# Optimization experiments

Measured on AMD Instinct MI355X. Metric: run time of the kernel, lower is better.

The kernel has to match this reference:

```python
import jax, jax.numpy as jnp
import numpy as np

NEG_INF = -9e15  # matches torch's -9000000000000000.0 mask value
ALPHA = 0.2      # LeakyReLU negative slope


def setup_inputs() -> dict:
    key = jax.random.key(0)
    k1, k2, k3, k4 = jax.random.split(key, 4)
    B, N, Fin, Fout = 8, 2048, 256, 256
    h = jax.random.normal(k1, (B, N, Fin), dtype=jnp.float32)
    adj = jax.random.randint(k2, (B, N, N), 0, 2, dtype=jnp.int32)
    # xavier_uniform with gain=1.414
    limW = 1.414 * np.sqrt(6.0 / (Fin + Fout))
    W = jax.random.uniform(k3, (Fin, Fout), minval=-limW, maxval=limW, dtype=jnp.float32)
    lima = 1.414 * np.sqrt(6.0 / (2 * Fout + 1))
    a = jax.random.uniform(k4, (2 * Fout, 1), minval=-lima, maxval=lima, dtype=jnp.float32)
    return {"h": h, "adj": adj, "W": W, "a": a}


def reference(h, adj, W, a):
    # h: (B, N, Fin), adj: (B, N, N), W: (Fin, Fout), a: (2*Fout, 1)
    Fout = W.shape[1]
    Wh = jnp.einsum('bni,io->bno', h, W)                 # (B, N, Fout)
    # e[b,i,j] = leakyrelu(Wh[b,i] @ a1 + Wh[b,j] @ a2) -- equivalent to the
    # original concat([Wh_i, Wh_j]) @ a without the O(N^2 * 2F) intermediate.
    e1 = Wh @ a[:Fout, 0]                                # (B, N)
    e2 = Wh @ a[Fout:, 0]                                # (B, N)
    e = jax.nn.leaky_relu(e1[:, :, None] + e2[:, None, :], negative_slope=ALPHA)
    masked = jnp.where(adj > 0, e, NEG_INF)
    attention = jax.nn.softmax(masked, axis=-1)          # (B, N, N)
    # dropout omitted (deterministic eval-mode reference)
    h_prime = jnp.einsum('bij,bjo->bio', attention, Wh)  # (B, N, Fout)
    return jax.nn.elu(h_prime), attention
```

## Files before the change

kernel.cpp:

```cpp
#include <hip/hip_runtime.h>
#include <hip/hip_bf16.h>
#include <stdint.h>

#define NEG_INF -9.0e15f
#define LRELU_ALPHA 0.2f
#define LOG2E 1.442695040888963f

using bf16x8  = __attribute__((ext_vector_type(8))) short;
using f32x4   = __attribute__((ext_vector_type(4))) float;
using short4v = __attribute__((ext_vector_type(4))) short;
using int4v   = __attribute__((ext_vector_type(4))) int;
using float4v = __attribute__((ext_vector_type(4))) float;
using uint2v  = __attribute__((ext_vector_type(2))) unsigned;
using uint4v  = __attribute__((ext_vector_type(4))) unsigned;

static __device__ __forceinline__ short f2bf(float f) {
  unsigned u = __builtin_bit_cast(unsigned, f);
  u = u + 0x7FFFu + ((u >> 16) & 1u);
  return (short)(u >> 16);
}
static __device__ __forceinline__ unsigned cvtpk_bf16(float lo, float hi) {
  unsigned r;
  asm volatile("v_cvt_pk_bf16_f32 %0, %1, %2" : "=v"(r) : "v"(lo), "v"(hi));
  return r;
}
static __device__ __forceinline__ void gload16(const void* g, void* l) {
  __builtin_amdgcn_global_load_lds((const __attribute__((address_space(1))) void*)g,
                                   (__attribute__((address_space(3))) void*)l, 16, 0, 0);
}

__global__ __launch_bounds__(256) void prep_kernel(
    const float* __restrict__ W, const float* __restrict__ a,
    short* __restrict__ W_t, float* __restrict__ aW1, float* __restrict__ aW2)
{
  const int bid = blockIdx.x;
  const int tid = threadIdx.x;
  if (bid < 16) {
    __shared__ float t[64][65];
    const int m0 = (bid & 3) * 64, n0 = (bid >> 2) * 64;
    const int rr = tid >> 3, cc = (tid & 7) * 8;
#pragma unroll
    for (int p = 0; p < 2; ++p) {
      int row = rr + p * 32;
      const float* sp = W + (m0 + row) * 256 + n0 + cc;
      float4v v0 = *(const float4v*)sp;
      float4v v1 = *(const float4v*)(sp + 4);
#pragma unroll
      for (int j = 0; j < 4; ++j) { t[row][cc + j] = v0[j]; t[row][cc + 4 + j] = v1[j]; }
    }
    __syncthreads();
#pragma unroll
    for (int p = 0; p < 2; ++p) {
      int orow = rr + p * 32;
      short vv[8] __attribute__((aligned(16)));
#pragma unroll
      for (int j = 0; j < 8; ++j) vv[j] = f2bf(t[cc + j][orow]);
      short* dp = W_t + (n0 + orow) * 256 + m0 + cc;
      *(int4v*)dp = *(const int4v*)vv;
    }
  } else {
    const int r8 = tid >> 3, o4 = (tid & 7) * 4;
    float s1[8] = {}, s2[8] = {};
#pragma unroll
    for (int rp = 0; rp < 8; ++rp) {
      int row = r8 + rp * 32;
#pragma unroll
      for (int k = 0; k < 8; ++k) {
        int o = o4 + k * 32;
        float4v wv = *(const float4v*)(W + row * 256 + o);
        float4v a1 = *(const float4v*)(a + o);
        float4v a2 = *(const float4v*)(a + 256 + o);
#pragma unroll
        for (int e = 0; e < 4; ++e) { s1[rp] += wv[e] * a1[e]; s2[rp] += wv[e] * a2[e]; }
      }
    }
#pragma unroll
    for (int rp = 0; rp < 8; ++rp) {
#pragma unroll
      for (int off = 4; off > 0; off >>= 1) {
        s1[rp] += __shfl_xor(s1[rp], off, 64);
        s2[rp] += __shfl_xor(s2[rp], off, 64);
      }
      if ((tid & 7) == 0) { aW1[r8 + rp * 32] = s1[rp]; aW2[r8 + rp * 32] = s2[rp]; }
    }
  }
}

__global__ __launch_bounds__(256) void gemm_h_kernel(
    const float* __restrict__ A, const short* __restrict__ Bt,
    short* __restrict__ Wht, const float* __restrict__ aW1,
    const float* __restrict__ aW2, float* __restrict__ e1, float* __restrict__ e2)
{
  __shared__ short As[128 * 32];
  __shared__ short Bs[128 * 32];
  __shared__ short T[128][136];
  const int m0 = blockIdx.x * 128, n0 = blockIdx.y * 128;
  const int tid = threadIdx.x;
  const int w = tid >> 6, lane = tid & 63;
  const int wr = w >> 1, wc = w & 1;
  const int g = lane >> 4, lr = lane & 15;
  const bool doE = (blockIdx.y == 0);

  f32x4 acc[4][4] = {};
  float s1q[2] = {0.f, 0.f}, s2q[2] = {0.f, 0.f};

  for (int k0 = 0; k0 < 256; k0 += 32) {
    __syncthreads();
#pragma unroll
    for (int q = 0; q < 2; ++q) {
      int c = q * 256 + tid;
      int row = c >> 2, kq = (c & 3) << 3;
      const float* ap = A + (long long)(m0 + row) * 256 + k0 + kq;
      float4v u0 = *(const float4v*)ap;
      float4v u1 = *(const float4v*)(ap + 4);
      if (doE) {
        float4v w1a = *(const float4v*)(aW1 + k0 + kq);
        float4v w1b = *(const float4v*)(aW1 + k0 + kq + 4);
        float4v w2a = *(const float4v*)(aW2 + k0 + kq);
        float4v w2b = *(const float4v*)(aW2 + k0 + kq + 4);
#pragma unroll
        for (int e = 0; e < 4; ++e) {
          s1q[q] += u0[e] * w1a[e] + u1[e] * w1b[e];
          s2q[q] += u0[e] * w2a[e] + u1[e] * w2b[e];
        }
      }
      uint4v uv;
      uv[0] = cvtpk_bf16(u0[0], u0[1]);
      uv[1] = cvtpk_bf16(u0[2], u0[3]);
      uv[2] = cvtpk_bf16(u1[0], u1[1]);
      uv[3] = cvtpk_bf16(u1[2], u1[3]);
      *(bf16x8*)(As + c * 8) = __builtin_bit_cast(bf16x8, uv);
    }
#pragma unroll
    for (int q = 0; q < 2; ++q) {
      int p = w * 2 + q;
      int c = p * 64 + lane;
      int row = c >> 2, kq = (c & 3) << 3;
      gload16(Bt + (long long)(n0 + row) * 256 + k0 + kq, Bs + p * 512);
    }
    __syncthreads();

    bf16x8 af[4], bfr[4];
#pragma unroll
    for (int i = 0; i < 4; ++i) {
      af[i]  = *(const bf16x8*)(As + (wr * 64 + i * 16 + lr) * 32 + 8 * g);
      bfr[i] = *(const bf16x8*)(Bs + (wc * 64 + i * 16 + lr) * 32 + 8 * g);
    }
#pragma unroll
    for (int i = 0; i < 4; ++i)
#pragma unroll
      for (int j = 0; j < 4; ++j)
        acc[i][j] = __builtin_amdgcn_mfma_f32_16x16x32_bf16(af[i], bfr[j], acc[i][j], 0, 0, 0);
  }

  if (doE) {
#pragma unroll
    for (int q = 0; q < 2; ++q) {
      float a1 = s1q[q], a2 = s2q[q];
      a1 += __shfl_xor(a1, 1, 64); a1 += __shfl_xor(a1, 2, 64);
      a2 += __shfl_xor(a2, 1, 64); a2 += __shfl_xor(a2, 2, 64);
      if ((tid & 3) == 0) {
        int row = m0 + q * 64 + (tid >> 2);
        e1[row] = a1; e2[row] = a2;
      }
    }
  }

  __syncthreads();
#pragma unroll
  for (int i = 0; i < 4; ++i) {
    int row_base = wr * 64 + i * 16 + 4 * g;
#pragma unroll
    for (int j = 0; j < 4; ++j) {
      int col = wc * 64 + j * 16 + lr;
#pragma unroll
      for (int r = 0; r < 4; ++r)
        T[col][row_base + r] = f2bf(acc[i][j][r]);
    }
  }
  __syncthreads();
  const int b = m0 >> 11, mloc = m0 & 2047;
  short* wb = Wht + (long long)b * 524288 + mloc;
#pragma unroll
  for (int p = 0; p < 8; ++p) {
    int c = (tid >> 4) + p * 16;
    int off = (tid & 15) * 8;
    bf16x8 v = *(const bf16x8*)(&T[c][off]);
    *(bf16x8*)(wb + (long long)(n0 + c) * 2048 + off) = v;
  }
}

__global__ __launch_bounds__(256) void pack_stats_kernel(
    const int* __restrict__ adj, const float* __restrict__ e1,
    const float* __restrict__ e2, unsigned char* __restrict__ mask,
    float* __restrict__ Lr, float* __restrict__ Dr)
{
  const int i = blockIdx.x;
  const int b = blockIdx.y;
  const long long row = (long long)b * 2048 + i;
  const int tid = threadIdx.x;
  const int wid = tid >> 6, lane = tid & 63;
  const int j0 = tid * 8;

  const int*   arow = adj + row * 2048 + j0;
  const float  ei   = e1[row];
  const float* e2b  = e2 + b * 2048 + j0;

  int4v   a0 = *(const int4v*)(arow);
  int4v   a1 = *(const int4v*)(arow + 4);
  float4v f0 = *(const float4v*)(e2b);
  float4v f1 = *(const float4v*)(e2b + 4);

  float s[8]; unsigned byte = 0u;
#pragma unroll
  for (int k = 0; k < 8; ++k) {
    float x = ei + (k < 4 ? f0[k] : f1[k - 4]);
    float v = fmaxf(x, LRELU_ALPHA * x);
    int  ad = (k < 4 ? a0[k] : a1[k - 4]);
    if (ad > 0) { s[k] = v; byte |= (1u << k); } else s[k] = NEG_INF;
  }
  float m = s[0];
#pragma unroll
  for (int k = 1; k < 8; ++k) m = fmaxf(m, s[k]);
#pragma unroll
  for (int off = 32; off > 0; off >>= 1) m = fmaxf(m, __shfl_xor(m, off, 64));

  __shared__ float wmax[4], wsum[4];
  if (lane == 0) wmax[wid] = m;
  __syncthreads();
  const float M = fmaxf(fmaxf(wmax[0], wmax[1]), fmaxf(wmax[2], wmax[3]));
  const bool empty = (M == NEG_INF);

  mask[row * 256 + tid] = empty ? (unsigned char)0xFF : (unsigned char)byte;

  float t = 0.f;
#pragma unroll
  for (int k = 0; k < 8; ++k) t += __expf(s[k] - M);
#pragma unroll
  for (int off = 32; off > 0; off >>= 1) t += __shfl_xor(t, off, 64);
  if (lane == 0) wsum[wid] = t;
  __syncthreads();
  if (tid == 0) {
    const float S = wsum[0] + wsum[1] + wsum[2] + wsum[3];
    Lr[row] = empty ? 0.0f : LOG2E;
    Dr[row] = empty ? -11.0f : (-M * LOG2E - __log2f(S));
  }
}

__global__ __launch_bounds__(256, 3) void pv_kernel(
    const unsigned char* __restrict__ mask, const float* __restrict__ e1,
    const float* __restrict__ e2, const float* __restrict__ Lr,
    const float* __restrict__ Dr, const short* __restrict__ Bt,
    float* __restrict__ attnw, float* __restrict__ C)
{
  __shared__ short As0[32 * 32],  As1[32 * 32];
  __shared__ short Bs0[256 * 32], Bs1[256 * 32];
  __shared__ float e2s[2048];
  __shared__ unsigned char msk[32 * 256];
  const int bid = blockIdx.x;
  const int bz  = bid & 7;
  const int M0  = (bid >> 3) << 5;
  const int tid = threadIdx.x;
  const int w = tid >> 6, lane = tid & 63;
  const int g = lane >> 4, lr = lane & 15;

  const long long rb = (long long)bz * 2048;
  Bt    += (long long)bz * 524288;
  attnw += (long long)bz * 4194304;
  C     += (long long)bz * 524288;

  const int pr = tid >> 3, k4 = (tid & 7) << 2;
  const int prow = M0 + pr;
  const float E1p = e1[rb + prow];
  const float Lp  = Lr[rb + prow];
  const float Dp  = Dr[rb + prow];
  float* arow = attnw + (long long)prow * 2048;
  const int kc = k4 >> 3;
  const int as_off = pr * 32 + ((kc ^ ((pr >> 1) & 3)) << 3) + (k4 & 7);

  const int bcol_off = lane >> 2;
  const int bchunk   = (lane & 3) ^ ((lane >> 3) & 3);

  {
    const float* e2g = e2 + rb;
    const unsigned char* mg = mask + (rb + M0) * 256;
#pragma unroll
    for (int q = 0; q < 2; ++q) {
      int p = w * 2 + q;
      gload16(e2g + p * 256 + lane * 4, (char*)e2s + p * 1024);
      gload16(mg  + p * 1024 + lane * 16, (char*)msk + p * 1024);
    }
  }

  f32x4 acc[2][4] = {};

  auto STAGE = [&](short* BsD, short* AsD, int k0) {
#pragma unroll
    for (int q = 0; q < 4; ++q) {
      int pp = w * 4 + q;
      int col = pp * 16 + bcol_off;
      gload16(Bt + (long long)col * 2048 + k0 + bchunk * 8, BsD + pp * 512);
    }
    const int kk = k0 + k4;
    const unsigned by = (unsigned)(msk[pr * 256 + (kk >> 3)] >> (k4 & 7)) & 0xFu;
    float4v ev = *(const float4v*)(e2s + kk);
    float p4[4];
#pragma unroll
    for (int e = 0; e < 4; ++e) {
      float x = E1p + ev[e];
      float v = fmaxf(x, LRELU_ALPHA * x);
      float P = __builtin_amdgcn_exp2f(fmaf(v, Lp, Dp));
      p4[e] = ((by >> e) & 1u) ? P : 0.0f;
    }
    float4v o;
#pragma unroll
    for (int e = 0; e < 4; ++e) o[e] = p4[e];
    *(float4v*)(arow + kk) = o;
    uint2v uv;
    uv[0] = cvtpk_bf16(p4[0], p4[1]);
    uv[1] = cvtpk_bf16(p4[2], p4[3]);
    *(uint2v*)(AsD + as_off) = uv;
  };

  auto COMPUTE = [&](const short* BsD, const short* AsD) {
    bf16x8 af[2], bfr[4];
#pragma unroll
    for (int i = 0; i < 2; ++i) {
      int row = i * 16 + lr;
      af[i] = *(const bf16x8*)(AsD + row * 32 + ((g ^ ((row >> 1) & 3)) << 3));
    }
#pragma unroll
    for (int j = 0; j < 4; ++j) {
      int col = w * 64 + j * 16 + lr;
      bfr[j] = *(const bf16x8*)(BsD + col * 32 + ((g ^ ((col >> 1) & 3)) << 3));
    }
#pragma unroll
    for (int i = 0; i < 2; ++i)
#pragma unroll
      for (int j = 0; j < 4; ++j)
        acc[i][j] = __builtin_amdgcn_mfma_f32_16x16x32_bf16(af[i], bfr[j], acc[i][j], 0, 0, 0);
  };

  __syncthreads();
  STAGE(Bs0, As0, 0);
  __syncthreads();
  for (int t = 0; t < 64; t += 2) {
    STAGE(Bs1, As1, (t + 1) * 32);
    COMPUTE(Bs0, As0);
    __syncthreads();
    if (t + 2 < 64) STAGE(Bs0, As0, (t + 2) * 32);
    COMPUTE(Bs1, As1);
    __syncthreads();
  }

#pragma unroll
  for (int i = 0; i < 2; ++i) {
    int row_base = M0 + i * 16 + 4 * g;
#pragma unroll
    for (int j = 0; j < 4; ++j) {
      int col = w * 64 + j * 16 + lr;
#pragma unroll
      for (int r = 0; r < 4; ++r) {
        float v = acc[i][j][r];
        v = (v > 0.f) ? v : (__expf(v) - 1.f);
        C[(long long)(row_base + r) * 256 + col] = v;
      }
    }
  }
}

extern "C" void kernel_launch(void* const* d_in, const int* in_sizes, int n_in,
                              void* d_out, int out_size, void* d_ws, size_t ws_size,
                              hipStream_t stream)
{
  const float* h   = (const float*)d_in[0];
  const int*   adj = (const int*)d_in[1];
  const float* W   = (const float*)d_in[2];
  const float* a   = (const float*)d_in[3];

  float* hp_out   = (float*)d_out;
  float* attn_out = hp_out + 4194304LL;

  unsigned char* mask = (unsigned char*)d_ws;
  short* W_t  = (short*)(mask + 4194304);
  short* Wh_t = W_t + 65536;
  float* e1   = (float*)(Wh_t + 4194304);
  float* e2   = e1 + 16384;
  float* Lr   = e2 + 16384;
  float* Dr   = Lr + 16384;
  float* aW1  = Dr + 16384;
  float* aW2  = aW1 + 256;

  prep_kernel<<<17, 256, 0, stream>>>(W, a, W_t, aW1, aW2);
  gemm_h_kernel<<<dim3(128, 2), 256, 0, stream>>>(h, W_t, Wh_t, aW1, aW2, e1, e2);
  pack_stats_kernel<<<dim3(2048, 8), 256, 0, stream>>>(adj, e1, e2, mask, Lr, Dr);
  pv_kernel<<<512, 256, 0, stream>>>(mask, e1, e2, Lr, Dr, Wh_t, attn_out, hp_out);
}
```

Before: 109.3 us.

## Fuse adjacency mask packing and softmax row stats into the PV kernel

Removes the separate pack_stats kernel. Each PV block now reads its 32 rows of adj directly, builds the bitmask in shared memory, and computes the row max and exp-sum with intra-row shuffles before the MFMA loop. This removes a kernel launch and the round trip of the byte mask and the Lr/Dr stats through global memory. In exchange the adj read (128MB) and a second exp pass move into the prologue of a 512-block kernel, where they may be less well parallelised than in the 16K-block kernel they replace, and they add register pressure.

```diff
diff --git a/kernel.cpp b/kernel.cpp
--- a/kernel.cpp
+++ b/kernel.cpp
@@ -190,73 +190,15 @@
   }
 }
 
-__global__ __launch_bounds__(256) void pack_stats_kernel(
+__global__ __launch_bounds__(256, 3) void fused_pv_kernel(
     const int* __restrict__ adj, const float* __restrict__ e1,
-    const float* __restrict__ e2, unsigned char* __restrict__ mask,
-    float* __restrict__ Lr, float* __restrict__ Dr)
-{
-  const int i = blockIdx.x;
-  const int b = blockIdx.y;
-  const long long row = (long long)b * 2048 + i;
-  const int tid = threadIdx.x;
-  const int wid = tid >> 6, lane = tid & 63;
-  const int j0 = tid * 8;
-
-  const int*   arow = adj + row * 2048 + j0;
-  const float  ei   = e1[row];
-  const float* e2b  = e2 + b * 2048 + j0;
-
-  int4v   a0 = *(const int4v*)(arow);
-  int4v   a1 = *(const int4v*)(arow + 4);
-  float4v f0 = *(const float4v*)(e2b);
-  float4v f1 = *(const float4v*)(e2b + 4);
-
-  float s[8]; unsigned byte = 0u;
-#pragma unroll
-  for (int k = 0; k < 8; ++k) {
-    float x = ei + (k < 4 ? f0[k] : f1[k - 4]);
-    float v = fmaxf(x, LRELU_ALPHA * x);
-    int  ad = (k < 4 ? a0[k] : a1[k - 4]);
-    if (ad > 0) { s[k] = v; byte |= (1u << k); } else s[k] = NEG_INF;
-  }
-  float m = s[0];
-#pragma unroll
-  for (int k = 1; k < 8; ++k) m = fmaxf(m, s[k]);
-#pragma unroll
-  for (int off = 32; off > 0; off >>= 1) m = fmaxf(m, __shfl_xor(m, off, 64));
-
-  __shared__ float wmax[4], wsum[4];
-  if (lane == 0) wmax[wid] = m;
-  __syncthreads();
-  const float M = fmaxf(fmaxf(wmax[0], wmax[1]), fmaxf(wmax[2], wmax[3]));
-  const bool empty = (M == NEG_INF);
-
-  mask[row * 256 + tid] = empty ? (unsigned char)0xFF : (unsigned char)byte;
-
-  float t = 0.f;
-#pragma unroll
-  for (int k = 0; k < 8; ++k) t += __expf(s[k] - M);
-#pragma unroll
-  for (int off = 32; off > 0; off >>= 1) t += __shfl_xor(t, off, 64);
-  if (lane == 0) wsum[wid] = t;
-  __syncthreads();
-  if (tid == 0) {
-    const float S = wsum[0] + wsum[1] + wsum[2] + wsum[3];
-    Lr[row] = empty ? 0.0f : LOG2E;
-    Dr[row] = empty ? -11.0f : (-M * LOG2E - __log2f(S));
-  }
-}
-
-__global__ __launch_bounds__(256, 3) void pv_kernel(
-    const unsigned char* __restrict__ mask, const float* __restrict__ e1,
-    const float* __restrict__ e2, const float* __restrict__ Lr,
-    const float* __restrict__ Dr, const short* __restrict__ Bt,
+    const float* __restrict__ e2, const short* __restrict__ Bt,
     float* __restrict__ attnw, float* __restrict__ C)
 {
   __shared__ short As0[32 * 32],  As1[32 * 32];
   __shared__ short Bs0[256 * 32], Bs1[256 * 32];
   __shared__ float e2s[2048];
-  __shared__ unsigned char msk[32 * 256];
+  __shared__ unsigned mskL[256 * 8];
   const int bid = blockIdx.x;
   const int bz  = bid & 7;
   const int M0  = (bid >> 3) << 5;
@@ -272,8 +214,6 @@
   const int pr = tid >> 3, k4 = (tid & 7) << 2;
   const int prow = M0 + pr;
   const float E1p = e1[rb + prow];
-  const float Lp  = Lr[rb + prow];
-  const float Dp  = Dr[rb + prow];
   float* arow = attnw + (long long)prow * 2048;
   const int kc = k4 >> 3;
   const int as_off = pr * 32 + ((kc ^ ((pr >> 1) & 3)) << 3) + (k4 & 7);
@@ -283,14 +223,73 @@
 
   {
     const float* e2g = e2 + rb;
-    const unsigned char* mg = mask + (rb + M0) * 256;
 #pragma unroll
     for (int q = 0; q < 2; ++q) {
       int p = w * 2 + q;
       gload16(e2g + p * 256 + lane * 4, (char*)e2s + p * 1024);
-      gload16(mg  + p * 1024 + lane * 16, (char*)msk + p * 1024);
-    }
-  }
+    }
+  }
+  __syncthreads();
+
+  const int* adjrow = adj + (rb + prow) * 2048 + k4;
+  unsigned b[8];
+  float vmax = NEG_INF;
+#pragma unroll
+  for (int u = 0; u < 8; ++u) {
+    unsigned bu = 0u;
+#pragma unroll
+    for (int s = 0; s < 8; ++s) {
+      const int t = u * 8 + s;
+      int4v   av = *(const int4v*)(adjrow + t * 32);
+      float4v ev = *(const float4v*)(e2s + t * 32 + k4);
+#pragma unroll
+      for (int e = 0; e < 4; ++e) {
+        float x = E1p + ev[e];
+        float v = fmaxf(x, LRELU_ALPHA * x);
+        if (av[e] > 0) { bu |= (1u << (s * 4 + e)); vmax = fmaxf(vmax, v); }
+      }
+    }
+    b[u] = bu;
+  }
+  unsigned anyb = b[0] | b[1] | b[2] | b[3] | b[4] | b[5] | b[6] | b[7];
+#pragma unroll
+  for (int off = 1; off < 8; off <<= 1) {
+    vmax = fmaxf(vmax, __shfl_xor(vmax, off, 64));
+    anyb |= (unsigned)__shfl_xor((int)anyb, off, 64);
+  }
+  const bool empty = (anyb == 0u);
+
+  float Lp, Dp;
+  if (empty) {
+#pragma unroll
+    for (int u = 0; u < 8; ++u) b[u] = 0xFFFFFFFFu;
+    Lp = 0.0f; Dp = -11.0f;
+  } else {
+    float S = 0.f;
+#pragma unroll
+    for (int u = 0; u < 8; ++u) {
+      if (!b[u]) continue;
+#pragma unroll
+      for (int s = 0; s < 8; ++s) {
+        const unsigned nib = (b[u] >> (s * 4)) & 0xFu;
+        if (!nib) continue;
+        const int t = u * 8 + s;
+        float4v ev = *(const float4v*)(e2s + t * 32 + k4);
+#pragma unroll
+        for (int e = 0; e < 4; ++e) {
+          float x = E1p + ev[e];
+          float v = fmaxf(x, LRELU_ALPHA * x);
+          float P = __builtin_amdgcn_exp2f((v - vmax) * LOG2E);
+          S += ((nib >> e) & 1u) ? P : 0.f;
+        }
+      }
+    }
+#pragma unroll
+    for (int off = 1; off < 8; off <<= 1) S += __shfl_xor(S, off, 64);
+    Lp = LOG2E; Dp = -vmax * LOG2E - __log2f(S);
+  }
+#pragma unroll
+  for (int u = 0; u < 8; ++u) mskL[tid * 8 + u] = b[u];
 
   f32x4 acc[2][4] = {};
 
@@ -301,8 +300,9 @@
       int col = pp * 16 + bcol_off;
       gload16(Bt + (long long)col * 2048 + k0 + bchunk * 8, BsD + pp * 512);
     }
+    const int t  = k0 >> 5;
     const int kk = k0 + k4;
-    const unsigned by = (unsigned)(msk[pr * 256 + (kk >> 3)] >> (k4 & 7)) & 0xFu;
+    const unsigned by = (mskL[tid * 8 + (t >> 3)] >> ((t & 7) * 4)) & 0xFu;
     float4v ev = *(const float4v*)(e2s + kk);
     float p4[4];
 #pragma unroll
@@ -341,7 +341,6 @@
         acc[i][j] = __builtin_amdgcn_mfma_f32_16x16x32_bf16(af[i], bfr[j], acc[i][j], 0, 0, 0);
   };
 
-  __syncthreads();
   STAGE(Bs0, As0, 0);
   __syncthreads();
   for (int t = 0; t < 64; t += 2) {
@@ -381,18 +380,17 @@
   float* hp_out   = (float*)d_out;
   float* attn_out = hp_out + 4194304LL;
 
-  unsigned char* mask = (unsigned char*)d_ws;
-  short* W_t  = (short*)(mask + 4194304);
+  short* W_t  = (short*)((unsigned char*)d_ws + 4194304);
   short* Wh_t = W_t + 65536;
   float* e1   = (float*)(Wh_t + 4194304);
   float* e2   = e1 + 16384;
-  float* Lr   = e2 + 16384;
-  float* Dr   = Lr + 16384;
-  float* aW1  = Dr + 16384;
+  float* Lr_unused = e2 + 16384;
+  float* Dr_unused = Lr_unused + 16384;
+  float* aW1  = Dr_unused + 16384;
   float* aW2  = aW1 + 256;
+  (void)Lr_unused; (void)Dr_unused;
 
   prep_kernel<<<17, 256, 0, stream>>>(W, a, W_t, aW1, aW2);
   gemm_h_kernel<<<dim3(128, 2), 256, 0, stream>>>(h, W_t, Wh_t, aW1, aW2, e1, e2);
-  pack_stats_kernel<<<dim3(2048, 8), 256, 0, stream>>>(adj, e1, e2, mask, Lr, Dr);
-  pv_kernel<<<512, 256, 0, stream>>>(mask, e1, e2, Lr, Dr, Wh_t, attn_out, hp_out);
-}
+  fused_pv_kernel<<<512, 256, 0, stream>>>(adj, e1, e2, Wh_t, attn_out, hp_out);
+}
```

Result: slower. 132.3 us (+21.1%).

## Precompute normalized bf16 probabilities in pack pass, stage into attention output rows

Applied to the files above, without the earlier changes.

The stats pass now computes the full normalized softmax row and stores it as bf16 in the upper half of each fp32 attention output row, used as scratch. The PV kernel no longer recomputes exp from a bitmask and row stats. It loads the bf16 probabilities straight into shared memory, widens them to fp32 for the attention output, and feeds them to MFMA. This drops the mask, the Lr/Dr buffers and the per-element exp work in the PV kernel, and raises occupancy to 4 blocks. The cost is extra global traffic for the bf16 staging, attention values rounded to bf16, and in-place overwriting of the scratch area, which relies on read-before-write ordering within each row.

```diff
diff --git a/kernel.cpp b/kernel.cpp
--- a/kernel.cpp
+++ b/kernel.cpp
@@ -190,10 +190,9 @@
   }
 }
 
-__global__ __launch_bounds__(256) void pack_stats_kernel(
+__global__ __launch_bounds__(256) void pack_kernel(
     const int* __restrict__ adj, const float* __restrict__ e1,
-    const float* __restrict__ e2, unsigned char* __restrict__ mask,
-    float* __restrict__ Lr, float* __restrict__ Dr)
+    const float* __restrict__ e2, float* __restrict__ attn)
 {
   const int i = blockIdx.x;
   const int b = blockIdx.y;
@@ -211,13 +210,13 @@
   float4v f0 = *(const float4v*)(e2b);
   float4v f1 = *(const float4v*)(e2b + 4);
 
-  float s[8]; unsigned byte = 0u;
+  float s[8];
 #pragma unroll
   for (int k = 0; k < 8; ++k) {
     float x = ei + (k < 4 ? f0[k] : f1[k - 4]);
     float v = fmaxf(x, LRELU_ALPHA * x);
     int  ad = (k < 4 ? a0[k] : a1[k - 4]);
-    if (ad > 0) { s[k] = v; byte |= (1u << k); } else s[k] = NEG_INF;
+    s[k] = (ad > 0) ? v : NEG_INF;
   }
   float m = s[0];
 #pragma unroll
@@ -229,34 +228,31 @@
   if (lane == 0) wmax[wid] = m;
   __syncthreads();
   const float M = fmaxf(fmaxf(wmax[0], wmax[1]), fmaxf(wmax[2], wmax[3]));
-  const bool empty = (M == NEG_INF);
-
-  mask[row * 256 + tid] = empty ? (unsigned char)0xFF : (unsigned char)byte;
-
-  float t = 0.f;
-#pragma unroll
-  for (int k = 0; k < 8; ++k) t += __expf(s[k] - M);
+
+  float p[8]; float t = 0.f;
+#pragma unroll
+  for (int k = 0; k < 8; ++k) { p[k] = __expf(s[k] - M); t += p[k]; }
 #pragma unroll
   for (int off = 32; off > 0; off >>= 1) t += __shfl_xor(t, off, 64);
   if (lane == 0) wsum[wid] = t;
   __syncthreads();
-  if (tid == 0) {
-    const float S = wsum[0] + wsum[1] + wsum[2] + wsum[3];
-    Lr[row] = empty ? 0.0f : LOG2E;
-    Dr[row] = empty ? -11.0f : (-M * LOG2E - __log2f(S));
-  }
-}
-
-__global__ __launch_bounds__(256, 3) void pv_kernel(
-    const unsigned char* __restrict__ mask, const float* __restrict__ e1,
-    const float* __restrict__ e2, const float* __restrict__ Lr,
-    const float* __restrict__ Dr, const short* __restrict__ Bt,
-    float* __restrict__ attnw, float* __restrict__ C)
+  const float S = wsum[0] + wsum[1] + wsum[2] + wsum[3];
+  const float r = 1.0f / S;
+
+  uint4v uv;
+  uv[0] = cvtpk_bf16(p[0] * r, p[1] * r);
+  uv[1] = cvtpk_bf16(p[2] * r, p[3] * r);
+  uv[2] = cvtpk_bf16(p[4] * r, p[5] * r);
+  uv[3] = cvtpk_bf16(p[6] * r, p[7] * r);
+  short* op = (short*)(attn + row * 2048 + 1024) + j0;
+  *(uint4v*)op = uv;
+}
+
+__global__ __launch_bounds__(256, 4) void pv_kernel(
+    const short* __restrict__ Bt, float* __restrict__ attnw, float* __restrict__ C)
 {
   __shared__ short As0[32 * 32],  As1[32 * 32];
   __shared__ short Bs0[256 * 32], Bs1[256 * 32];
-  __shared__ float e2s[2048];
-  __shared__ unsigned char msk[32 * 256];
   const int bid = blockIdx.x;
   const int bz  = bid & 7;
   const int M0  = (bid >> 3) << 5;
@@ -264,33 +260,22 @@
   const int w = tid >> 6, lane = tid & 63;
   const int g = lane >> 4, lr = lane & 15;
 
-  const long long rb = (long long)bz * 2048;
   Bt    += (long long)bz * 524288;
   attnw += (long long)bz * 4194304;
   C     += (long long)bz * 524288;
 
   const int pr = tid >> 3, k4 = (tid & 7) << 2;
-  const int prow = M0 + pr;
-  const float E1p = e1[rb + prow];
-  const float Lp  = Lr[rb + prow];
-  const float Dp  = Dr[rb + prow];
-  float* arow = attnw + (long long)prow * 2048;
   const int kc = k4 >> 3;
   const int as_off = pr * 32 + ((kc ^ ((pr >> 1) & 3)) << 3) + (k4 & 7);
+  float* arow = attnw + (long long)(M0 + pr) * 2048;
 
   const int bcol_off = lane >> 2;
   const int bchunk   = (lane & 3) ^ ((lane >> 3) & 3);
 
-  {
-    const float* e2g = e2 + rb;
-    const unsigned char* mg = mask + (rb + M0) * 256;
-#pragma unroll
-    for (int q = 0; q < 2; ++q) {
-      int p = w * 2 + q;
-      gload16(e2g + p * 256 + lane * 4, (char*)e2s + p * 1024);
-      gload16(mg  + p * 1024 + lane * 16, (char*)msk + p * 1024);
-    }
-  }
+  const int a_s  = w * 64 + lane;
+  const int a_r  = a_s >> 2, a_cs = a_s & 3;
+  const int a_dc = a_cs ^ ((a_r >> 1) & 3);
+  const short* aP = (const short*)(attnw + (long long)(M0 + a_r) * 2048 + 1024) + a_dc * 8;
 
   f32x4 acc[2][4] = {};
 
@@ -301,28 +286,18 @@
       int col = pp * 16 + bcol_off;
       gload16(Bt + (long long)col * 2048 + k0 + bchunk * 8, BsD + pp * 512);
     }
-    const int kk = k0 + k4;
-    const unsigned by = (unsigned)(msk[pr * 256 + (kk >> 3)] >> (k4 & 7)) & 0xFu;
-    float4v ev = *(const float4v*)(e2s + kk);
-    float p4[4];
-#pragma unroll
-    for (int e = 0; e < 4; ++e) {
-      float x = E1p + ev[e];
-      float v = fmaxf(x, LRELU_ALPHA * x);
-      float P = __builtin_amdgcn_exp2f(fmaf(v, Lp, Dp));
-      p4[e] = ((by >> e) & 1u) ? P : 0.0f;
-    }
+    if (w < 2) gload16(aP + k0, AsD + w * 512);
+  };
+
+  auto COMPUTE = [&](const short* BsD, const short* AsD, int k0) {
+    uint2v pw = *(const uint2v*)(AsD + as_off);
     float4v o;
-#pragma unroll
-    for (int e = 0; e < 4; ++e) o[e] = p4[e];
-    *(float4v*)(arow + kk) = o;
-    uint2v uv;
-    uv[0] = cvtpk_bf16(p4[0], p4[1]);
-    uv[1] = cvtpk_bf16(p4[2], p4[3]);
-    *(uint2v*)(AsD + as_off) = uv;
-  };
-
-  auto COMPUTE = [&](const short* BsD, const short* AsD) {
+    o[0] = __builtin_bit_cast(float, pw[0] << 16);
+    o[1] = __builtin_bit_cast(float, pw[0] & 0xFFFF0000u);
+    o[2] = __builtin_bit_cast(float, pw[1] << 16);
+    o[3] = __builtin_bit_cast(float, pw[1] & 0xFFFF0000u);
+    *(float4v*)(arow + k0 + k4) = o;
+
     bf16x8 af[2], bfr[4];
 #pragma unroll
     for (int i = 0; i < 2; ++i) {
@@ -341,15 +316,14 @@
         acc[i][j] = __builtin_amdgcn_mfma_f32_16x16x32_bf16(af[i], bfr[j], acc[i][j], 0, 0, 0);
   };
 
-  __syncthreads();
   STAGE(Bs0, As0, 0);
   __syncthreads();
   for (int t = 0; t < 64; t += 2) {
     STAGE(Bs1, As1, (t + 1) * 32);
-    COMPUTE(Bs0, As0);
+    COMPUTE(Bs0, As0, t * 32);
     __syncthreads();
     if (t + 2 < 64) STAGE(Bs0, As0, (t + 2) * 32);
-    COMPUTE(Bs1, As1);
+    COMPUTE(Bs1, As1, (t + 1) * 32);
     __syncthreads();
   }
 
@@ -381,18 +355,15 @@
   float* hp_out   = (float*)d_out;
   float* attn_out = hp_out + 4194304LL;
 
-  unsigned char* mask = (unsigned char*)d_ws;
-  short* W_t  = (short*)(mask + 4194304);
+  short* W_t  = (short*)d_ws;
   short* Wh_t = W_t + 65536;
   float* e1   = (float*)(Wh_t + 4194304);
   float* e2   = e1 + 16384;
-  float* Lr   = e2 + 16384;
-  float* Dr   = Lr + 16384;
-  float* aW1  = Dr + 16384;
+  float* aW1  = e2 + 16384;
   float* aW2  = aW1 + 256;
 
   prep_kernel<<<17, 256, 0, stream>>>(W, a, W_t, aW1, aW2);
   gemm_h_kernel<<<dim3(128, 2), 256, 0, stream>>>(h, W_t, Wh_t, aW1, aW2, e1, e2);
-  pack_stats_kernel<<<dim3(2048, 8), 256, 0, stream>>>(adj, e1, e2, mask, Lr, Dr);
-  pv_kernel<<<512, 256, 0, stream>>>(mask, e1, e2, Lr, Dr, Wh_t, attn_out, hp_out);
-}
+  pack_kernel<<<dim3(2048, 8), 256, 0, stream>>>(adj, e1, e2, attn_out);
+  pv_kernel<<<512, 256, 0, stream>>>(Wh_t, attn_out, hp_out);
+}
```

Measured after the change: 121.9 us. +11.5%, slower.
